# Kernel optimization log

Measured on AMD Instinct MI355X. Metric: run time of the kernel, lower is better.

## Reference

```python
import jax, jax.numpy as jnp
import numpy as np

B, N, F = 4, 2048, 256
NEG = -9e15

def setup_inputs() -> dict:
    key = jax.random.key(0)
    k1, k2, k3, k4 = jax.random.split(key, 4)
    x = jax.random.normal(k1, (B, N, F), dtype=jnp.float32)
    adj = jax.random.randint(k2, (B, N, N), 0, 2, dtype=jnp.int32)
    W = jax.random.normal(k3, (F, F), dtype=jnp.float32) * 0.07
    a = jax.random.normal(k4, (2 * F, 1), dtype=jnp.float32) * 0.07
    return {"x": x, "adj": adj, "W": W, "a": a}

def reference(x, adj, W, a):
    # h = (x @ W): [B, N, F]
    h = jnp.einsum('bnf,fg->bng', x, W)
    # Pairwise score e_ij = relu(a^T [h_i ; h_j]) decomposed to avoid the
    # O(N^2 * 2F) concat tensor (same math as the torch repeat/cat version).
    f_src = h @ a[:F, 0]   # [B, N]  contribution of h_i
    f_dst = h @ a[F:, 0]   # [B, N]  contribution of h_j
    e = jax.nn.relu(f_src[:, :, None] + f_dst[:, None, :])  # [B, N, N]
    att = jnp.where(adj > 0, e, NEG)
    att = jax.nn.softmax(att, axis=2)
    # dropout is identity in eval mode (training=False)
    h_prime = jnp.einsum('bnm,bmf->bnf', att, h)
    return jax.nn.elu(h_prime)  # concat=True -> elu
```

## Files before the change

kernel.cpp:

```cpp
#include <hip/hip_runtime.h>
#include <hip/hip_bf16.h>

#define NB 4
#define NN 2048
#define NF 256
#define LOG2E 1.4426950408889634f

using bf16x8 = __attribute__((ext_vector_type(8))) short;
using f32x4  = __attribute__((ext_vector_type(4))) float;

__device__ __forceinline__ short f2bf(float f) {
    unsigned u = __float_as_uint(f);
    u += 0x7fffu + ((u >> 16) & 1u);
    return (short)(u >> 16);
}
__device__ __forceinline__ unsigned enc_ord(float f) {
    unsigned u = __float_as_uint(f);
    return (u & 0x80000000u) ? ~u : (u | 0x80000000u);
}
__device__ __forceinline__ float dec_ord(unsigned u) {
    unsigned i = (u & 0x80000000u) ? (u & 0x7fffffffu) : ~u;
    return __uint_as_float(i);
}
__device__ __forceinline__ void gll16(const void* g, void* l) {
    __builtin_amdgcn_global_load_lds(
        (const __attribute__((address_space(1))) unsigned int*)g,
        (__attribute__((address_space(3))) unsigned int*)l, 16, 0, 0);
}

__global__ __launch_bounds__(256) void prep_kernel(
    const float* __restrict__ W, short* __restrict__ WT, unsigned* __restrict__ maxfd)
{
    const int blk = blockIdx.x, tid = threadIdx.x;
    if (blk < (NF*NF)/256) {
        int t = blk*256 + tid;
        WT[t] = f2bf(W[(t & 255)*NF + (t >> 8)]);
    } else if (tid < NB) {
        maxfd[tid] = 0u;
    }
}

__global__ __launch_bounds__(256,4) void work2_kernel(
    const int* __restrict__ adj, unsigned short* __restrict__ adjB16,
    const float* __restrict__ x, const short* __restrict__ WT, const float* __restrict__ a,
    short* __restrict__ hT, float* __restrict__ fs2, float* __restrict__ fd2,
    unsigned* __restrict__ maxfd)
{
    if (blockIdx.x >= 512) {
        const int g = (blockIdx.x - 512)*256 + threadIdx.x;
        const int4* p = (const int4*)(adj + (size_t)g*16);
        int4 v0 = p[0], v1 = p[1], v2 = p[2], v3 = p[3];
        unsigned m = 0;
        m |= (v0.x>0)<<0;  m |= (v0.y>0)<<1;  m |= (v0.z>0)<<2;  m |= (v0.w>0)<<3;
        m |= (v1.x>0)<<4;  m |= (v1.y>0)<<5;  m |= (v1.z>0)<<6;  m |= (v1.w>0)<<7;
        m |= (v2.x>0)<<8;  m |= (v2.y>0)<<9;  m |= (v2.z>0)<<10; m |= (v2.w>0)<<11;
        m |= (v3.x>0)<<12; m |= (v3.y>0)<<13; m |= (v3.z>0)<<14; m |= (v3.w>0)<<15;
        adjB16[g] = (unsigned short)m;
        return;
    }
    __shared__ float fs_l[16], fd_l[16];
    const int hb = blockIdx.x;
    const int w  = threadIdx.x >> 6;
    const int l  = threadIdx.x & 63;
    const int lr = l & 15, lg = l >> 4;
    const int b  = hb >> 7;
    const int ib = (hb & 127) * 16;

    if (threadIdx.x < 16) { fs_l[threadIdx.x] = 0.f; fd_l[threadIdx.x] = 0.f; }
    __syncthreads();

    f32x4 acc[4];
    #pragma unroll
    for (int t = 0; t < 4; t++) acc[t] = (f32x4){0.f,0.f,0.f,0.f};

    const float* xrow = x + (size_t)(b*NN + ib + lr) * NF + 8*lg;
    const short* wtp  = WT + (size_t)(w*64 + lr) * NF + 8*lg;

    float4 xa[2][2]; bf16x8 bfr[2][4];
    xa[0][0] = *(const float4*)(xrow);
    xa[0][1] = *(const float4*)(xrow + 4);
    #pragma unroll
    for (int nt = 0; nt < 4; nt++) bfr[0][nt] = *(const bf16x8*)(wtp + nt*16*NF);

    #pragma unroll
    for (int ks = 0; ks < 8; ks++) {
        const int cur = ks & 1;
        if (ks < 7) {
            const int nxt = cur ^ 1;
            xa[nxt][0] = *(const float4*)(xrow + (ks+1)*32);
            xa[nxt][1] = *(const float4*)(xrow + (ks+1)*32 + 4);
            #pragma unroll
            for (int nt = 0; nt < 4; nt++)
                bfr[nxt][nt] = *(const bf16x8*)(wtp + nt*16*NF + (ks+1)*32);
        }
        bf16x8 af;
        af[0]=f2bf(xa[cur][0].x); af[1]=f2bf(xa[cur][0].y);
        af[2]=f2bf(xa[cur][0].z); af[3]=f2bf(xa[cur][0].w);
        af[4]=f2bf(xa[cur][1].x); af[5]=f2bf(xa[cur][1].y);
        af[6]=f2bf(xa[cur][1].z); af[7]=f2bf(xa[cur][1].w);
        #pragma unroll
        for (int nt = 0; nt < 4; nt++)
            acc[nt] = __builtin_amdgcn_mfma_f32_16x16x32_bf16(af, bfr[cur][nt], acc[nt], 0, 0, 0);
    }

    float fsv[4] = {0,0,0,0}, fdv[4] = {0,0,0,0};
    #pragma unroll
    for (int nt = 0; nt < 4; nt++) {
        int g = w*64 + nt*16 + lr;
        float as = a[g], ad = a[NF + g];
        short4 hv;
        hv.x = f2bf(acc[nt][0]); hv.y = f2bf(acc[nt][1]);
        hv.z = f2bf(acc[nt][2]); hv.w = f2bf(acc[nt][3]);
        *(short4*)(hT + ((size_t)(b*NF + g))*NN + ib + lg*4) = hv;
        #pragma unroll
        for (int r = 0; r < 4; r++) { fsv[r] += acc[nt][r]*as; fdv[r] += acc[nt][r]*ad; }
    }
    #pragma unroll
    for (int mask = 1; mask < 16; mask <<= 1) {
        #pragma unroll
        for (int r = 0; r < 4; r++) {
            fsv[r] += __shfl_xor(fsv[r], mask);
            fdv[r] += __shfl_xor(fdv[r], mask);
        }
    }
    if (lr == 0) {
        #pragma unroll
        for (int r = 0; r < 4; r++) {
            atomicAdd(&fs_l[lg*4 + r], fsv[r]);
            atomicAdd(&fd_l[lg*4 + r], fdv[r]);
        }
    }
    __syncthreads();
    if (threadIdx.x < 16) {
        float fsu = fs_l[threadIdx.x] * LOG2E;
        float fdu = fd_l[threadIdx.x] * LOG2E;
        fs2[b*NN + ib + threadIdx.x] = fsu;
        fd2[b*NN + ib + threadIdx.x] = fdu;
        float wm = fdu;
        #pragma unroll
        for (int m = 1; m < 16; m <<= 1) wm = fmaxf(wm, __shfl_xor(wm, m));
        if (threadIdx.x == 0) atomicMax(maxfd + b, enc_ord(wm));
    }
}

__global__ __launch_bounds__(512,4) void gat_fused(
    const short* __restrict__ hT, const unsigned char* __restrict__ adjB,
    const float* __restrict__ fs2, const float* __restrict__ fd2,
    const unsigned* __restrict__ maxfd, float* __restrict__ out)
{
    __shared__ __align__(16) char smem[65536];

    const int tid = threadIdx.x;
    const int w = tid >> 6, l = tid & 63, lr = l & 15, lg = l >> 4;
    const int kt = w & 3, rowg = w >> 2;
    const int blk = blockIdx.x;
    const int b = blk >> 7, rest = blk & 127;
    const int itile = rest >> 1, fh = rest & 1;
    const int i0 = itile * 32, f0 = fh * 128;

    const short* hTb = hT + ((size_t)b * NF + f0) * NN;

    const short* sbp[4];
    #pragma unroll
    for (int i = 0; i < 4; ++i) {
        int s = tid + 512*i;
        int r = s >> 4, pc = s & 15;
        int c = pc ^ (r & 15);
        sbp[i] = hTb + (size_t)r * NN + c*8;
    }

    const float mx2 = dec_ord(maxfd[b]);
    const int gi = b*NN + i0 + rowg*16 + lr;
    const float fsv_ = fs2[gi];
    const float M = fmaxf(fsv_ + mx2, 0.f);
    const float fsM = fsv_ - M, nM = -M;

    const unsigned char* ar = adjB + (size_t)gi * (NN/8) + kt*4 + lg;
    const float* fdp = fd2 + b*NN + kt*32 + lg*8;

    const int boff = lr*256 + (((kt*4 + lg) ^ lr) << 4);

    f32x4 acc[8];
    #pragma unroll
    for (int j = 0; j < 8; ++j) acc[j] = (f32x4){0.f,0.f,0.f,0.f};
    f32x4 acc1 = (f32x4){0.f,0.f,0.f,0.f};

    bf16x8 bONE;
    #pragma unroll
    for (int d = 0; d < 8; ++d) bONE[d] = (short)0x3F80;

    auto STAGE = [&](int t, int slot) {
        char* dst = smem + slot * 32768;
        #pragma unroll
        for (int i = 0; i < 4; ++i)
            gll16(sbp[i] + t*128, dst + (tid + 512*i)*16);
    };
    auto LOADP = [&](int t, unsigned& m8, f32x4& fa, f32x4& fb) {
        m8 = ar[t*16];
        fa = *(const f32x4*)(fdp + (t << 7));
        fb = *(const f32x4*)(fdp + (t << 7) + 4);
    };
    auto BODY = [&](int slot, unsigned m8, const f32x4& fa, const f32x4& fb) {
        const char* sb = smem + slot * 32768;
        bf16x8 B[8];
        #pragma unroll
        for (int nt = 0; nt < 8; ++nt)
            B[nt] = *(const bf16x8*)(sb + boff + nt*4096);
        const float fdv[8] = {fa[0],fa[1],fa[2],fa[3],fb[0],fb[1],fb[2],fb[3]};
        float p[8];
        #pragma unroll
        for (int e = 0; e < 8; ++e) {
            float v = __builtin_amdgcn_exp2f(fmaxf(fsM + fdv[e], nM));
            p[e] = (m8 & (1u << e)) ? v : 0.f;
        }
        union { bf16x8 v; unsigned u[4]; } au;
        #pragma unroll
        for (int d = 0; d < 4; ++d)
            asm("v_cvt_pk_bf16_f32 %0, %1, %2" : "=v"(au.u[d]) : "v"(p[2*d]), "v"(p[2*d+1]));
        #pragma unroll
        for (int nt = 0; nt < 8; ++nt)
            acc[nt] = __builtin_amdgcn_mfma_f32_16x16x32_bf16(au.v, B[nt], acc[nt], 0, 0, 0);
        acc1 = __builtin_amdgcn_mfma_f32_16x16x32_bf16(au.v, bONE, acc1, 0, 0, 0);
    };
    #define FENCE3 do { __builtin_amdgcn_sched_barrier(0); \
        asm volatile("s_waitcnt vmcnt(3)" ::: "memory"); \
        __builtin_amdgcn_s_barrier(); \
        __builtin_amdgcn_sched_barrier(0); } while (0)
    #define FENCE0 do { __builtin_amdgcn_sched_barrier(0); \
        asm volatile("s_waitcnt vmcnt(0)" ::: "memory"); \
        __builtin_amdgcn_s_barrier(); \
        __builtin_amdgcn_sched_barrier(0); } while (0)

    unsigned mA, mB;
    f32x4 fAa, fAb, fBa, fBb;

    STAGE(0, 0);
    LOADP(0, mA, fAa, fAb);
    LOADP(1, mB, fBa, fBb);
    FENCE3;

    for (int t2 = 0; t2 < 16; t2 += 2) {
        STAGE(t2 + 1, 1);
        BODY(0, mA, fAa, fAb);
        if (t2 + 2 < 16) {
            LOADP(t2 + 2, mA, fAa, fAb);
            FENCE3;
        } else {
            FENCE0;
        }
        if (t2 + 2 < 16) STAGE(t2 + 2, 0);
        BODY(1, mB, fBa, fBb);
        if (t2 + 3 < 16) {
            LOADP(t2 + 3, mB, fBa, fBb);
            FENCE3;
        }
    }
    __syncthreads();

    float* red0 = (float*)smem;
    float* red1 = (float*)(smem + 16896);
    float* myr0 = red0 + rowg * 16*132;
    float* myr1 = red1 + rowg * 16*132;
    if (kt >= 2) {
        float* dst = (kt == 2) ? myr0 : myr1;
        #pragma unroll
        for (int nt = 0; nt < 8; ++nt)
            #pragma unroll
            for (int r = 0; r < 4; ++r)
                dst[(lg*4 + r)*132 + nt*16 + lr] = acc[nt][r];
        if (lr == 0)
            #pragma unroll
            for (int r = 0; r < 4; ++r)
                dst[(lg*4 + r)*132 + 128] = acc1[r];
    }
    __syncthreads();
    if (kt < 2) {
        const float* srcp = (kt == 0) ? myr0 : myr1;
        #pragma unroll
        for (int nt = 0; nt < 8; ++nt)
            #pragma unroll
            for (int r = 0; r < 4; ++r)
                acc[nt][r] += srcp[(lg*4 + r)*132 + nt*16 + lr];
        #pragma unroll
        for (int r = 0; r < 4; ++r)
            acc1[r] += srcp[(lg*4 + r)*132 + 128];
    }
    __syncthreads();
    if (kt == 1) {
        #pragma unroll
        for (int nt = 0; nt < 8; ++nt)
            #pragma unroll
            for (int r = 0; r < 4; ++r)
                myr0[(lg*4 + r)*132 + nt*16 + lr] = acc[nt][r];
        if (lr == 0)
            #pragma unroll
            for (int r = 0; r < 4; ++r)
                myr0[(lg*4 + r)*132 + 128] = acc1[r];
    }
    __syncthreads();
    if (kt == 0) {
        float rv[4];
        #pragma unroll
        for (int r = 0; r < 4; ++r) {
            float tot = acc1[r] + myr0[(lg*4 + r)*132 + 128];
            rv[r] = tot > 0.f ? 1.f / tot : 0.f;
        }
        #pragma unroll
        for (int nt = 0; nt < 8; ++nt)
            #pragma unroll
            for (int r = 0; r < 4; ++r) {
                float v = acc[nt][r] + myr0[(lg*4 + r)*132 + nt*16 + lr];
                v *= rv[r];
                v = v > 0.f ? v : expm1f(v);
                int row = i0 + rowg*16 + lg*4 + r;
                out[(size_t)(b*NN + row)*NF + f0 + nt*16 + lr] = v;
            }
    }
    #undef FENCE3
    #undef FENCE0
}

extern "C" void kernel_launch(void* const* d_in, const int* in_sizes, int n_in,
                              void* d_out, int out_size, void* d_ws, size_t ws_size,
                              hipStream_t stream) {
    const float* x   = (const float*)d_in[0];
    const int*   adj = (const int*)d_in[1];
    const float* W   = (const float*)d_in[2];
    const float* a   = (const float*)d_in[3];
    float* out = (float*)d_out;
    char* ws = (char*)d_ws;

    short* WT       = (short*)(ws);
    short* hT       = (short*)(ws + 0x20000);
    float* fs2      = (float*)(ws + 0x420000);
    float* fd2      = (float*)(ws + 0x428000);
    unsigned* maxfd = (unsigned*)(ws + 0x430000);
    unsigned short* adjB16 = (unsigned short*)(ws + 0x440000);

    prep_kernel<<<(NF*NF)/256 + 1, 256, 0, stream>>>(W, WT, maxfd);
    work2_kernel<<<4608, 256, 0, stream>>>(adj, adjB16, x, WT, a,
                                           hT, fs2, fd2, maxfd);
    gat_fused<<<NB*128, 512, 0, stream>>>(hT, (const unsigned char*)adjB16,
                                          fs2, fd2, maxfd, out);
}
```

Before: 61.18 us.

## Halve fused kernel block to 256 threads with 2-way K split and remap blocks

The fused attention kernel moves from 8 waves (4-way K split) to 4 waves (2-way K split). Each K stage now covers 64 columns instead of 128, so there are twice as many pipeline iterations, with half the LDS per stage and a smaller swizzle. The cross-wave reduction drops from two rounds to one, and LDS use halves, which may allow more resident blocks per CU. Block indices are also permuted to interleave work across XCDs, though each block now carries a longer serial loop.

Result: slower. 63.36 us (+3.6%).

```diff
diff --git a/kernel.cpp b/kernel.cpp
--- a/kernel.cpp
+++ b/kernel.cpp
@@ -143,18 +143,18 @@
     }
 }
 
-__global__ __launch_bounds__(512,4) void gat_fused(
+__global__ __launch_bounds__(256,4) void gat_fused(
     const short* __restrict__ hT, const unsigned char* __restrict__ adjB,
     const float* __restrict__ fs2, const float* __restrict__ fd2,
     const unsigned* __restrict__ maxfd, float* __restrict__ out)
 {
-    __shared__ __align__(16) char smem[65536];
+    __shared__ __align__(16) char smem[33792];
 
     const int tid = threadIdx.x;
     const int w = tid >> 6, l = tid & 63, lr = l & 15, lg = l >> 4;
-    const int kt = w & 3, rowg = w >> 2;
-    const int blk = blockIdx.x;
-    const int b = blk >> 7, rest = blk & 127;
+    const int kt = w & 1, rowg = w >> 1;
+    const int wg = ((blockIdx.x & 7) << 6) | (blockIdx.x >> 3);
+    const int b = wg >> 7, rest = wg & 127;
     const int itile = rest >> 1, fh = rest & 1;
     const int i0 = itile * 32, f0 = fh * 128;
 
@@ -163,9 +163,9 @@
     const short* sbp[4];
     #pragma unroll
     for (int i = 0; i < 4; ++i) {
-        int s = tid + 512*i;
-        int r = s >> 4, pc = s & 15;
-        int c = pc ^ (r & 15);
+        int s = tid + 256*i;
+        int r = s >> 3, pc = s & 7;
+        int c = pc ^ (r & 7);
         sbp[i] = hTb + (size_t)r * NN + c*8;
     }
 
@@ -178,7 +178,7 @@
     const unsigned char* ar = adjB + (size_t)gi * (NN/8) + kt*4 + lg;
     const float* fdp = fd2 + b*NN + kt*32 + lg*8;
 
-    const int boff = lr*256 + (((kt*4 + lg) ^ lr) << 4);
+    const int boff = lr*128 + (((kt*4 + lg) ^ (lr & 7)) << 4);
 
     f32x4 acc[8];
     #pragma unroll
@@ -190,22 +190,22 @@
     for (int d = 0; d < 8; ++d) bONE[d] = (short)0x3F80;
 
     auto STAGE = [&](int t, int slot) {
-        char* dst = smem + slot * 32768;
+        char* dst = smem + slot * 16384;
         #pragma unroll
         for (int i = 0; i < 4; ++i)
-            gll16(sbp[i] + t*128, dst + (tid + 512*i)*16);
+            gll16(sbp[i] + t*64, dst + (tid + 256*i)*16);
     };
     auto LOADP = [&](int t, unsigned& m8, f32x4& fa, f32x4& fb) {
-        m8 = ar[t*16];
-        fa = *(const f32x4*)(fdp + (t << 7));
-        fb = *(const f32x4*)(fdp + (t << 7) + 4);
+        m8 = ar[t*8];
+        fa = *(const f32x4*)(fdp + (t << 6));
+        fb = *(const f32x4*)(fdp + (t << 6) + 4);
     };
     auto BODY = [&](int slot, unsigned m8, const f32x4& fa, const f32x4& fb) {
-        const char* sb = smem + slot * 32768;
+        const char* sb = smem + slot * 16384;
         bf16x8 B[8];
         #pragma unroll
         for (int nt = 0; nt < 8; ++nt)
-            B[nt] = *(const bf16x8*)(sb + boff + nt*4096);
+            B[nt] = *(const bf16x8*)(sb + boff + nt*2048);
         const float fdv[8] = {fa[0],fa[1],fa[2],fa[3],fb[0],fb[1],fb[2],fb[3]};
         float p[8];
         #pragma unroll
@@ -239,77 +239,50 @@
     LOADP(1, mB, fBa, fBb);
     FENCE3;
 
-    for (int t2 = 0; t2 < 16; t2 += 2) {
+    for (int t2 = 0; t2 < 32; t2 += 2) {
         STAGE(t2 + 1, 1);
         BODY(0, mA, fAa, fAb);
-        if (t2 + 2 < 16) {
+        if (t2 + 2 < 32) {
             LOADP(t2 + 2, mA, fAa, fAb);
             FENCE3;
         } else {
             FENCE0;
         }
-        if (t2 + 2 < 16) STAGE(t2 + 2, 0);
+        if (t2 + 2 < 32) STAGE(t2 + 2, 0);
         BODY(1, mB, fBa, fBb);
-        if (t2 + 3 < 16) {
+        if (t2 + 3 < 32) {
             LOADP(t2 + 3, mB, fBa, fBb);
             FENCE3;
         }
     }
     __syncthreads();
 
-    float* red0 = (float*)smem;
-    float* red1 = (float*)(smem + 16896);
-    float* myr0 = red0 + rowg * 16*132;
-    float* myr1 = red1 + rowg * 16*132;
-    if (kt >= 2) {
-        float* dst = (kt == 2) ? myr0 : myr1;
+    float* red = (float*)smem;
+    float* myr = red + rowg * 16*132;
+    if (kt == 1) {
         #pragma unroll
         for (int nt = 0; nt < 8; ++nt)
             #pragma unroll
             for (int r = 0; r < 4; ++r)
-                dst[(lg*4 + r)*132 + nt*16 + lr] = acc[nt][r];
+                myr[(lg*4 + r)*132 + nt*16 + lr] = acc[nt][r];
         if (lr == 0)
             #pragma unroll
             for (int r = 0; r < 4; ++r)
-                dst[(lg*4 + r)*132 + 128] = acc1[r];
-    }
-    __syncthreads();
-    if (kt < 2) {
-        const float* srcp = (kt == 0) ? myr0 : myr1;
-        #pragma unroll
-        for (int nt = 0; nt < 8; ++nt)
-            #pragma unroll
-            for (int r = 0; r < 4; ++r)
-                acc[nt][r] += srcp[(lg*4 + r)*132 + nt*16 + lr];
-        #pragma unroll
-        for (int r = 0; r < 4; ++r)
-            acc1[r] += srcp[(lg*4 + r)*132 + 128];
-    }
-    __syncthreads();
-    if (kt == 1) {
-        #pragma unroll
-        for (int nt = 0; nt < 8; ++nt)
-            #pragma unroll
-            for (int r = 0; r < 4; ++r)
-                myr0[(lg*4 + r)*132 + nt*16 + lr] = acc[nt][r];
-        if (lr == 0)
-            #pragma unroll
-            for (int r = 0; r < 4; ++r)
-                myr0[(lg*4 + r)*132 + 128] = acc1[r];
+                myr[(lg*4 + r)*132 + 128] = acc1[r];
     }
     __syncthreads();
     if (kt == 0) {
         float rv[4];
         #pragma unroll
         for (int r = 0; r < 4; ++r) {
-            float tot = acc1[r] + myr0[(lg*4 + r)*132 + 128];
+            float tot = acc1[r] + myr[(lg*4 + r)*132 + 128];
             rv[r] = tot > 0.f ? 1.f / tot : 0.f;
         }
         #pragma unroll
         for (int nt = 0; nt < 8; ++nt)
             #pragma unroll
             for (int r = 0; r < 4; ++r) {
-                float v = acc[nt][r] + myr0[(lg*4 + r)*132 + nt*16 + lr];
+                float v = acc[nt][r] + myr[(lg*4 + r)*132 + nt*16 + lr];
                 v *= rv[r];
                 v = v > 0.f ? v : expm1f(v);
                 int row = i0 + rowg*16 + lg*4 + r;
@@ -340,6 +313,6 @@
     prep_kernel<<<(NF*NF)/256 + 1, 256, 0, stream>>>(W, WT, maxfd);
     work2_kernel<<<4608, 256, 0, stream>>>(adj, adjB16, x, WT, a,
                                            hT, fs2, fd2, maxfd);
-    gat_fused<<<NB*128, 512, 0, stream>>>(hT, (const unsigned char*)adjB16,
+    gat_fused<<<NB*128, 256, 0, stream>>>(hT, (const unsigned char*)adjB16,
                                           fs2, fd2, maxfd, out);
 }
```

## Switch aggregation to 32x32x16 MFMA with 8-way k-split and scalar rowsum

Applied to the files above, without the earlier changes.

Replaces the 16x16x32 MFMA tiling (two row groups by four k-splits plus a ones-vector MFMA for the softmax denominator) with 32x32x16 MFMAs, where each of the eight waves covers all 32 rows and a k-slice. The row sum is now accumulated in scalar registers and reduced through a shuffle and LDS, which removes the extra MFMA per step. The cross-wave reduction becomes a three-level tree over eight partials. This cuts MFMA issue count and B-fragment LDS reads, at the cost of more reduction passes through LDS and more barriers in the epilogue.

Result: slower. 69.68 us (+13.9%).

```diff
diff --git a/kernel.cpp b/kernel.cpp
--- a/kernel.cpp
+++ b/kernel.cpp
@@ -8,6 +8,7 @@
 
 using bf16x8 = __attribute__((ext_vector_type(8))) short;
 using f32x4  = __attribute__((ext_vector_type(4))) float;
+using f32x16 = __attribute__((ext_vector_type(16))) float;
 
 __device__ __forceinline__ short f2bf(float f) {
     unsigned u = __float_as_uint(f);
@@ -148,11 +149,10 @@
     const float* __restrict__ fs2, const float* __restrict__ fd2,
     const unsigned* __restrict__ maxfd, float* __restrict__ out)
 {
-    __shared__ __align__(16) char smem[65536];
+    __shared__ __align__(16) char smem[66560];
 
     const int tid = threadIdx.x;
-    const int w = tid >> 6, l = tid & 63, lr = l & 15, lg = l >> 4;
-    const int kt = w & 3, rowg = w >> 2;
+    const int kt = tid >> 6, l = tid & 63, fr = l & 31, h = l >> 5;
     const int blk = blockIdx.x;
     const int b = blk >> 7, rest = blk & 127;
     const int itile = rest >> 1, fh = rest & 1;
@@ -170,24 +170,18 @@
     }
 
     const float mx2 = dec_ord(maxfd[b]);
-    const int gi = b*NN + i0 + rowg*16 + lr;
+    const int gi = b*NN + i0 + fr;
     const float fsv_ = fs2[gi];
     const float M = fmaxf(fsv_ + mx2, 0.f);
     const float fsM = fsv_ - M, nM = -M;
 
-    const unsigned char* ar = adjB + (size_t)gi * (NN/8) + kt*4 + lg;
-    const float* fdp = fd2 + b*NN + kt*32 + lg*8;
-
-    const int boff = lr*256 + (((kt*4 + lg) ^ lr) << 4);
-
-    f32x4 acc[8];
-    #pragma unroll
-    for (int j = 0; j < 8; ++j) acc[j] = (f32x4){0.f,0.f,0.f,0.f};
-    f32x4 acc1 = (f32x4){0.f,0.f,0.f,0.f};
-
-    bf16x8 bONE;
-    #pragma unroll
-    for (int d = 0; d < 8; ++d) bONE[d] = (short)0x3F80;
+    const unsigned char* ar = adjB + (size_t)gi * (NN/8) + kt*2 + h;
+    const float* fdp = fd2 + b*NN + kt*16 + h*8;
+
+    const int boff = fr*256 + (((kt*2 + h) ^ (fr & 15)) << 4);
+
+    f32x16 acc[4] = {};
+    float lsum = 0.f;
 
     auto STAGE = [&](int t, int slot) {
         char* dst = smem + slot * 32768;
@@ -202,25 +196,26 @@
     };
     auto BODY = [&](int slot, unsigned m8, const f32x4& fa, const f32x4& fb) {
         const char* sb = smem + slot * 32768;
-        bf16x8 B[8];
-        #pragma unroll
-        for (int nt = 0; nt < 8; ++nt)
-            B[nt] = *(const bf16x8*)(sb + boff + nt*4096);
+        bf16x8 B[4];
+        #pragma unroll
+        for (int ft = 0; ft < 4; ++ft)
+            B[ft] = *(const bf16x8*)(sb + boff + ft*8192);
         const float fdv[8] = {fa[0],fa[1],fa[2],fa[3],fb[0],fb[1],fb[2],fb[3]};
         float p[8];
         #pragma unroll
         for (int e = 0; e < 8; ++e) {
             float v = __builtin_amdgcn_exp2f(fmaxf(fsM + fdv[e], nM));
-            p[e] = (m8 & (1u << e)) ? v : 0.f;
+            v = (m8 & (1u << e)) ? v : 0.f;
+            lsum += v;
+            p[e] = v;
         }
         union { bf16x8 v; unsigned u[4]; } au;
         #pragma unroll
         for (int d = 0; d < 4; ++d)
             asm("v_cvt_pk_bf16_f32 %0, %1, %2" : "=v"(au.u[d]) : "v"(p[2*d]), "v"(p[2*d+1]));
         #pragma unroll
-        for (int nt = 0; nt < 8; ++nt)
-            acc[nt] = __builtin_amdgcn_mfma_f32_16x16x32_bf16(au.v, B[nt], acc[nt], 0, 0, 0);
-        acc1 = __builtin_amdgcn_mfma_f32_16x16x32_bf16(au.v, bONE, acc1, 0, 0, 0);
+        for (int ft = 0; ft < 4; ++ft)
+            acc[ft] = __builtin_amdgcn_mfma_f32_32x32x16_bf16(au.v, B[ft], acc[ft], 0, 0, 0);
     };
     #define FENCE3 do { __builtin_amdgcn_sched_barrier(0); \
         asm volatile("s_waitcnt vmcnt(3)" ::: "memory"); \
@@ -255,66 +250,59 @@
             FENCE3;
         }
     }
-    __syncthreads();
-
-    float* red0 = (float*)smem;
-    float* red1 = (float*)(smem + 16896);
-    float* myr0 = red0 + rowg * 16*132;
-    float* myr1 = red1 + rowg * 16*132;
-    if (kt >= 2) {
-        float* dst = (kt == 2) ? myr0 : myr1;
-        #pragma unroll
-        for (int nt = 0; nt < 8; ++nt)
+
+    lsum += __shfl_xor(lsum, 32);
+    __syncthreads();
+
+    float* ls = (float*)(smem + 65536);
+    if (h == 0) ls[fr*8 + kt] = lsum;
+
+    auto redbuf = [&](int q) { return (float*)(smem + q*16384); };
+    auto STORE = [&](float* dst) {
+        #pragma unroll
+        for (int ft = 0; ft < 4; ++ft)
             #pragma unroll
-            for (int r = 0; r < 4; ++r)
-                dst[(lg*4 + r)*132 + nt*16 + lr] = acc[nt][r];
-        if (lr == 0)
+            for (int reg = 0; reg < 16; ++reg) {
+                int row = (reg & 3) + 8*(reg >> 2) + 4*h;
+                dst[row*128 + ft*32 + fr] = acc[ft][reg];
+            }
+    };
+    auto ADD = [&](const float* src) {
+        #pragma unroll
+        for (int ft = 0; ft < 4; ++ft)
             #pragma unroll
-            for (int r = 0; r < 4; ++r)
-                dst[(lg*4 + r)*132 + 128] = acc1[r];
-    }
-    __syncthreads();
-    if (kt < 2) {
-        const float* srcp = (kt == 0) ? myr0 : myr1;
-        #pragma unroll
-        for (int nt = 0; nt < 8; ++nt)
+            for (int reg = 0; reg < 16; ++reg) {
+                int row = (reg & 3) + 8*(reg >> 2) + 4*h;
+                acc[ft][reg] += src[row*128 + ft*32 + fr];
+            }
+    };
+
+    if (kt >= 4) STORE(redbuf(kt - 4));
+    __syncthreads();
+    if (kt < 4) ADD(redbuf(kt));
+    __syncthreads();
+    if (kt == 2 || kt == 3) STORE(redbuf(kt - 2));
+    __syncthreads();
+    if (kt < 2) ADD(redbuf(kt));
+    __syncthreads();
+    if (kt == 1) STORE(redbuf(0));
+    __syncthreads();
+    if (kt == 0) {
+        ADD(redbuf(0));
+        #pragma unroll
+        for (int reg = 0; reg < 16; ++reg) {
+            int row = (reg & 3) + 8*(reg >> 2) + 4*h;
+            f32x4 s0 = *(const f32x4*)&ls[row*8];
+            f32x4 s1 = *(const f32x4*)&ls[row*8 + 4];
+            float tot = (s0[0]+s0[1]) + (s0[2]+s0[3]) + (s1[0]+s1[1]) + (s1[2]+s1[3]);
+            float rv = tot > 0.f ? 1.f / tot : 0.f;
             #pragma unroll
-            for (int r = 0; r < 4; ++r)
-                acc[nt][r] += srcp[(lg*4 + r)*132 + nt*16 + lr];
-        #pragma unroll
-        for (int r = 0; r < 4; ++r)
-            acc1[r] += srcp[(lg*4 + r)*132 + 128];
-    }
-    __syncthreads();
-    if (kt == 1) {
-        #pragma unroll
-        for (int nt = 0; nt < 8; ++nt)
-            #pragma unroll
-            for (int r = 0; r < 4; ++r)
-                myr0[(lg*4 + r)*132 + nt*16 + lr] = acc[nt][r];
-        if (lr == 0)
-            #pragma unroll
-            for (int r = 0; r < 4; ++r)
-                myr0[(lg*4 + r)*132 + 128] = acc1[r];
-    }
-    __syncthreads();
-    if (kt == 0) {
-        float rv[4];
-        #pragma unroll
-        for (int r = 0; r < 4; ++r) {
-            float tot = acc1[r] + myr0[(lg*4 + r)*132 + 128];
-            rv[r] = tot > 0.f ? 1.f / tot : 0.f;
-        }
-        #pragma unroll
-        for (int nt = 0; nt < 8; ++nt)
-            #pragma unroll
-            for (int r = 0; r < 4; ++r) {
-                float v = acc[nt][r] + myr0[(lg*4 + r)*132 + nt*16 + lr];
-                v *= rv[r];
+            for (int ft = 0; ft < 4; ++ft) {
+                float v = acc[ft][reg] * rv;
                 v = v > 0.f ? v : expm1f(v);
-                int row = i0 + rowg*16 + lg*4 + r;
-                out[(size_t)(b*NN + row)*NF + f0 + nt*16 + lr] = v;
+                out[(size_t)(b*NN + i0 + row)*NF + f0 + ft*32 + fr] = v;
             }
+        }
     }
     #undef FENCE3
     #undef FENCE0
```

## Give each wave private LDS staging to drop block barriers in main loop

Applied to the files above, without the earlier changes.

The fused attention kernel shrinks from 512 to 256 threads with 16-row tiles and doubles the grid. Each wave now stages only the hT slice for its own k-range into a private LDS region, so the per-step s_barrier goes away and only per-wave vmcnt waits remain. The softmax denominator partials move to a small separate LDS array for the final reduction. The cost is that the hT B-tiles are no longer shared across two row groups, which doubles global/L2 traffic for hT per output row. Occupancy also shifts, since each block now uses about 65 KB of LDS.

Measured after the change: 76.70 us. 1.25x slower.

```diff
diff --git a/kernel.cpp b/kernel.cpp
--- a/kernel.cpp
+++ b/kernel.cpp
@@ -143,34 +143,34 @@
     }
 }
 
-__global__ __launch_bounds__(512,4) void gat_fused(
+__global__ __launch_bounds__(256,2) void gat_fused(
     const short* __restrict__ hT, const unsigned char* __restrict__ adjB,
     const float* __restrict__ fs2, const float* __restrict__ fd2,
     const unsigned* __restrict__ maxfd, float* __restrict__ out)
 {
-    __shared__ __align__(16) char smem[65536];
+    __shared__ __align__(16) char smem[66560];
 
     const int tid = threadIdx.x;
-    const int w = tid >> 6, l = tid & 63, lr = l & 15, lg = l >> 4;
-    const int kt = w & 3, rowg = w >> 2;
+    const int kt = tid >> 6, l = tid & 63, lr = l & 15, lg = l >> 4;
     const int blk = blockIdx.x;
-    const int b = blk >> 7, rest = blk & 127;
+    const int b = blk >> 8, rest = blk & 255;
     const int itile = rest >> 1, fh = rest & 1;
-    const int i0 = itile * 32, f0 = fh * 128;
+    const int i0 = itile * 16, f0 = fh * 128;
 
     const short* hTb = hT + ((size_t)b * NF + f0) * NN;
-
-    const short* sbp[4];
-    #pragma unroll
-    for (int i = 0; i < 4; ++i) {
-        int s = tid + 512*i;
-        int r = s >> 4, pc = s & 15;
-        int c = pc ^ (r & 15);
-        sbp[i] = hTb + (size_t)r * NN + c*8;
+    char* wbase = smem + kt * 16384;
+
+    const short* sbp[8];
+    #pragma unroll
+    for (int i = 0; i < 8; ++i) {
+        int c = i*64 + l;
+        int r = c >> 2, q = c & 3;
+        int qs = q ^ ((r >> 1) & 3);
+        sbp[i] = hTb + (size_t)r * NN + kt*32 + qs*8;
     }
 
     const float mx2 = dec_ord(maxfd[b]);
-    const int gi = b*NN + i0 + rowg*16 + lr;
+    const int gi = b*NN + i0 + lr;
     const float fsv_ = fs2[gi];
     const float M = fmaxf(fsv_ + mx2, 0.f);
     const float fsM = fsv_ - M, nM = -M;
@@ -178,7 +178,7 @@
     const unsigned char* ar = adjB + (size_t)gi * (NN/8) + kt*4 + lg;
     const float* fdp = fd2 + b*NN + kt*32 + lg*8;
 
-    const int boff = lr*256 + (((kt*4 + lg) ^ lr) << 4);
+    const int boff = lr*64 + ((lg ^ ((lr >> 1) & 3)) << 4);
 
     f32x4 acc[8];
     #pragma unroll
@@ -190,10 +190,10 @@
     for (int d = 0; d < 8; ++d) bONE[d] = (short)0x3F80;
 
     auto STAGE = [&](int t, int slot) {
-        char* dst = smem + slot * 32768;
-        #pragma unroll
-        for (int i = 0; i < 4; ++i)
-            gll16(sbp[i] + t*128, dst + (tid + 512*i)*16);
+        char* dst = wbase + slot * 8192;
+        #pragma unroll
+        for (int i = 0; i < 8; ++i)
+            gll16(sbp[i] + t*128, dst + i*1024 + l*16);
     };
     auto LOADP = [&](int t, unsigned& m8, f32x4& fa, f32x4& fb) {
         m8 = ar[t*16];
@@ -201,11 +201,11 @@
         fb = *(const f32x4*)(fdp + (t << 7) + 4);
     };
     auto BODY = [&](int slot, unsigned m8, const f32x4& fa, const f32x4& fb) {
-        const char* sb = smem + slot * 32768;
+        const char* sb = wbase + slot * 8192;
         bf16x8 B[8];
         #pragma unroll
         for (int nt = 0; nt < 8; ++nt)
-            B[nt] = *(const bf16x8*)(sb + boff + nt*4096);
+            B[nt] = *(const bf16x8*)(sb + boff + nt*1024);
         const float fdv[8] = {fa[0],fa[1],fa[2],fa[3],fb[0],fb[1],fb[2],fb[3]};
         float p[8];
         #pragma unroll
@@ -222,13 +222,11 @@
             acc[nt] = __builtin_amdgcn_mfma_f32_16x16x32_bf16(au.v, B[nt], acc[nt], 0, 0, 0);
         acc1 = __builtin_amdgcn_mfma_f32_16x16x32_bf16(au.v, bONE, acc1, 0, 0, 0);
     };
-    #define FENCE3 do { __builtin_amdgcn_sched_barrier(0); \
-        asm volatile("s_waitcnt vmcnt(3)" ::: "memory"); \
-        __builtin_amdgcn_s_barrier(); \
+    #define FENCEW11 do { __builtin_amdgcn_sched_barrier(0); \
+        asm volatile("s_waitcnt vmcnt(11)" ::: "memory"); \
         __builtin_amdgcn_sched_barrier(0); } while (0)
-    #define FENCE0 do { __builtin_amdgcn_sched_barrier(0); \
+    #define FENCEW0 do { __builtin_amdgcn_sched_barrier(0); \
         asm volatile("s_waitcnt vmcnt(0)" ::: "memory"); \
-        __builtin_amdgcn_s_barrier(); \
         __builtin_amdgcn_sched_barrier(0); } while (0)
 
     unsigned mA, mB;
@@ -236,54 +234,53 @@
 
     STAGE(0, 0);
     LOADP(0, mA, fAa, fAb);
+    STAGE(1, 1);
     LOADP(1, mB, fBa, fBb);
-    FENCE3;
+    FENCEW11;
 
     for (int t2 = 0; t2 < 16; t2 += 2) {
-        STAGE(t2 + 1, 1);
         BODY(0, mA, fAa, fAb);
+        __builtin_amdgcn_sched_barrier(0);
         if (t2 + 2 < 16) {
+            STAGE(t2 + 2, 0);
             LOADP(t2 + 2, mA, fAa, fAb);
-            FENCE3;
+            FENCEW11;
         } else {
-            FENCE0;
-        }
-        if (t2 + 2 < 16) STAGE(t2 + 2, 0);
+            FENCEW0;
+        }
         BODY(1, mB, fBa, fBb);
+        __builtin_amdgcn_sched_barrier(0);
         if (t2 + 3 < 16) {
+            STAGE(t2 + 3, 1);
             LOADP(t2 + 3, mB, fBa, fBb);
-            FENCE3;
+            FENCEW11;
         }
     }
     __syncthreads();
 
     float* red0 = (float*)smem;
-    float* red1 = (float*)(smem + 16896);
-    float* myr0 = red0 + rowg * 16*132;
-    float* myr1 = red1 + rowg * 16*132;
+    float* red1 = (float*)(smem + 8448);
+    float* ls   = (float*)(smem + 16896);
+    if (lr == 0) {
+        #pragma unroll
+        for (int r = 0; r < 4; ++r) ls[(lg*4 + r)*4 + kt] = acc1[r];
+    }
     if (kt >= 2) {
-        float* dst = (kt == 2) ? myr0 : myr1;
+        float* dst = (kt == 2) ? red0 : red1;
         #pragma unroll
         for (int nt = 0; nt < 8; ++nt)
             #pragma unroll
             for (int r = 0; r < 4; ++r)
                 dst[(lg*4 + r)*132 + nt*16 + lr] = acc[nt][r];
-        if (lr == 0)
-            #pragma unroll
-            for (int r = 0; r < 4; ++r)
-                dst[(lg*4 + r)*132 + 128] = acc1[r];
     }
     __syncthreads();
     if (kt < 2) {
-        const float* srcp = (kt == 0) ? myr0 : myr1;
+        const float* srcp = (kt == 0) ? red0 : red1;
         #pragma unroll
         for (int nt = 0; nt < 8; ++nt)
             #pragma unroll
             for (int r = 0; r < 4; ++r)
                 acc[nt][r] += srcp[(lg*4 + r)*132 + nt*16 + lr];
-        #pragma unroll
-        for (int r = 0; r < 4; ++r)
-            acc1[r] += srcp[(lg*4 + r)*132 + 128];
     }
     __syncthreads();
     if (kt == 1) {
@@ -291,33 +288,30 @@
         for (int nt = 0; nt < 8; ++nt)
             #pragma unroll
             for (int r = 0; r < 4; ++r)
-                myr0[(lg*4 + r)*132 + nt*16 + lr] = acc[nt][r];
-        if (lr == 0)
-            #pragma unroll
-            for (int r = 0; r < 4; ++r)
-                myr0[(lg*4 + r)*132 + 128] = acc1[r];
+                red0[(lg*4 + r)*132 + nt*16 + lr] = acc[nt][r];
     }
     __syncthreads();
     if (kt == 0) {
         float rv[4];
         #pragma unroll
         for (int r = 0; r < 4; ++r) {
-            float tot = acc1[r] + myr0[(lg*4 + r)*132 + 128];
+            const float* lsr = ls + (lg*4 + r)*4;
+            float tot = (lsr[0] + lsr[1]) + (lsr[2] + lsr[3]);
             rv[r] = tot > 0.f ? 1.f / tot : 0.f;
         }
         #pragma unroll
         for (int nt = 0; nt < 8; ++nt)
             #pragma unroll
             for (int r = 0; r < 4; ++r) {
-                float v = acc[nt][r] + myr0[(lg*4 + r)*132 + nt*16 + lr];
+                float v = acc[nt][r] + red0[(lg*4 + r)*132 + nt*16 + lr];
                 v *= rv[r];
                 v = v > 0.f ? v : expm1f(v);
-                int row = i0 + rowg*16 + lg*4 + r;
+                int row = i0 + lg*4 + r;
                 out[(size_t)(b*NN + row)*NF + f0 + nt*16 + lr] = v;
             }
     }
-    #undef FENCE3
-    #undef FENCE0
+    #undef FENCEW11
+    #undef FENCEW0
 }
 
 extern "C" void kernel_launch(void* const* d_in, const int* in_sizes, int n_in,
@@ -340,6 +334,6 @@
     prep_kernel<<<(NF*NF)/256 + 1, 256, 0, stream>>>(W, WT, maxfd);
     work2_kernel<<<4608, 256, 0, stream>>>(adj, adjB16, x, WT, a,
                                            hT, fs2, fd2, maxfd);
-    gat_fused<<<NB*128, 512, 0, stream>>>(hT, (const unsigned char*)adjB16,
+    gat_fused<<<NB*256, 256, 0, stream>>>(hT, (const unsigned char*)adjB16,
                                           fs2, fd2, maxfd, out);
 }
```
